# Optimization experiments

Measured on AMD Instinct MI355X. Metric: run time of the kernel, lower is better.

Reference implementation:

```python
import jax, jax.numpy as jnp
import numpy as np

N_NODES = 100000
N_EDGES = 25000
NNZ = 800000
D_IN = 256
D_OUT = 256


def setup_inputs() -> dict:
    key = jax.random.key(0)
    k1, k2, k3, k4, k5, k6, k7 = jax.random.split(key, 7)
    return {
        "input": jax.random.normal(k1, (N_NODES, D_IN), dtype=jnp.float32),
        "V": jax.random.randint(k2, (NNZ,), 0, N_NODES, dtype=jnp.int32),
        "E": jax.random.randint(k3, (NNZ,), 0, N_EDGES, dtype=jnp.int32),
        "degV": jax.random.uniform(k4, (N_NODES, 1), dtype=jnp.float32),
        "degE": jax.random.uniform(k5, (N_EDGES, 1), dtype=jnp.float32),
        "weight": jax.random.normal(k6, (D_IN, D_OUT), dtype=jnp.float32) / np.sqrt(D_OUT),
        "bias": jax.random.normal(k7, (D_OUT,), dtype=jnp.float32) / np.sqrt(D_OUT),
    }


def reference(input, V, E, degV, degE, weight, bias):
    num_nodes = degV.shape[0]
    num_edges = degE.shape[0]
    # dense projection: [N, D_in] @ [D_in, D_out]
    X = input @ weight
    # vertex -> edge: gather per-incidence node feats, scatter-mean into edges
    Xve = X[V]  # [nnz, D_out]
    esum = jax.ops.segment_sum(Xve, E, num_segments=num_edges)
    ecnt = jax.ops.segment_sum(jnp.ones((E.shape[0], 1), X.dtype), E, num_segments=num_edges)
    Xe = esum / jnp.maximum(ecnt, 1.0)  # scatter mean
    Xe = Xe * degE  # edge degree scaling
    # edge -> vertex: gather edge feats, scatter-sum into nodes
    Xev = Xe[E]  # [nnz, D_out]
    Xv = jax.ops.segment_sum(Xev, V, num_segments=num_nodes)
    return Xv * degV + bias
```

## Files before the change

kernel.cpp:

```cpp
#include <hip/hip_runtime.h>
#include <stdint.h>

#define N_NODES 100000
#define N_EDGES 25000
#define NNZ_    800000
#define D       256
#define NTOT    (N_EDGES + N_NODES)
#define SB      1024
#define NBLK    ((NTOT + SB) / SB)
#define MP      25024

#define SHE   9
#define SHV   11
#define WKE   512
#define WKV   2048
#define NBKE  ((N_EDGES + WKE - 1) / WKE)
#define NBKV  ((N_NODES + WKV - 1) / WKV)
#define NB    (NBKE + NBKV)
#define CAP   24576

#define WB 256
#define CB ((N_NODES * D / 8 + 255) / 256)

typedef short  short8   __attribute__((ext_vector_type(8)));
typedef float  f32x4    __attribute__((ext_vector_type(4)));
typedef ushort ushortx8 __attribute__((ext_vector_type(8)));
typedef ushort ushortx4 __attribute__((ext_vector_type(4)));

__device__ __forceinline__ ushort f2bf(float f) {
    uint32_t u = __float_as_uint(f);
    uint32_t r = u + 0x7fffu + ((u >> 16) & 1u);
    return (ushort)(r >> 16);
}
__device__ __forceinline__ float bf2f(ushort u) {
    return __uint_as_float(((uint32_t)u) << 16);
}


__global__ void __launch_bounds__(256) front_kernel(const float* __restrict__ W,
                                                    ushort* __restrict__ WT,
                                                    const float* __restrict__ in,
                                                    ushort* __restrict__ Xbf) {
    int b = blockIdx.x, t = threadIdx.x;
    if (b < WB) {
        int g = b * 256 + t;
        int n = g >> 8, k = g & 255;
        WT[(size_t)n * 256 + k] = f2bf(W[(size_t)k * 256 + n]);
    } else {
        int i = (b - WB) * 256 + t;
        if (i >= N_NODES * D / 8) return;
        const float4* p = reinterpret_cast<const float4*>(in) + (size_t)i * 2;
        float4 a = p[0], c = p[1];
        ushortx8 o;
        o[0] = f2bf(a.x); o[1] = f2bf(a.y); o[2] = f2bf(a.z); o[3] = f2bf(a.w);
        o[4] = f2bf(c.x); o[5] = f2bf(c.y); o[6] = f2bf(c.z); o[7] = f2bf(c.w);
        *(reinterpret_cast<ushortx8*>(Xbf) + i) = o;
    }
}


__global__ void __launch_bounds__(256) scatter1(const int* __restrict__ V,
                                                const int* __restrict__ E,
                                                int* __restrict__ gcur,
                                                int2* __restrict__ pairs) {
    __shared__ int cnt[NB], base[NB], lcur[NB];
    int t = threadIdx.x;
    for (int j = t; j < NB; j += 256) cnt[j] = 0;
    __syncthreads();
    int i0 = (blockIdx.x * 256 + t) * 16;
    bool act = i0 < NNZ_;
    if (act) {
#pragma unroll
        for (int c = 0; c < 16; c += 4) {
            int4 e = *reinterpret_cast<const int4*>(E + i0 + c);
            int4 v = *reinterpret_cast<const int4*>(V + i0 + c);
            atomicAdd(&cnt[e.x >> SHE], 1);
            atomicAdd(&cnt[e.y >> SHE], 1);
            atomicAdd(&cnt[e.z >> SHE], 1);
            atomicAdd(&cnt[e.w >> SHE], 1);
            atomicAdd(&cnt[NBKE + (v.x >> SHV)], 1);
            atomicAdd(&cnt[NBKE + (v.y >> SHV)], 1);
            atomicAdd(&cnt[NBKE + (v.z >> SHV)], 1);
            atomicAdd(&cnt[NBKE + (v.w >> SHV)], 1);
        }
    }
    __syncthreads();
    for (int j = t; j < NB; j += 256) {
        int c = cnt[j];
        base[j] = c ? atomicAdd(&gcur[j], c) : 0;
        lcur[j] = 0;
    }
    __syncthreads();
    if (act) {
#pragma unroll
        for (int c = 0; c < 16; c += 4) {
            int4 e = *reinterpret_cast<const int4*>(E + i0 + c);
            int4 v = *reinterpret_cast<const int4*>(V + i0 + c);
            int ev[4] = {e.x, e.y, e.z, e.w};
            int vv[4] = {v.x, v.y, v.z, v.w};
#pragma unroll
            for (int k = 0; k < 4; ++k) {
                int b1 = ev[k] >> SHE;
                int p1 = base[b1] + atomicAdd(&lcur[b1], 1);
                if (p1 < CAP) pairs[(size_t)b1 * CAP + p1] = make_int2(ev[k], vv[k]);
                int b2 = NBKE + (vv[k] >> SHV);
                int p2 = base[b2] + atomicAdd(&lcur[b2], 1);
                if (p2 < CAP) pairs[(size_t)b2 * CAP + p2] = make_int2(vv[k], ev[k]);
            }
        }
    }
}


__global__ void __launch_bounds__(256) count2(const int2* __restrict__ pairs,
                                              const int* __restrict__ gcur,
                                              int* __restrict__ cntC) {
    __shared__ int hist[WKV];
    int b = blockIdx.x, t = threadIdx.x;
    bool eside = b < NBKE;
    int kb    = eside ? b * WKE : (b - NBKE) * WKV;
    int wk    = eside ? WKE : WKV;
    int nk    = eside ? min(WKE, N_EDGES - kb) : min(WKV, N_NODES - kb);
    int obase = eside ? kb : N_EDGES + kb;
    for (int j = t; j < wk; j += 256) hist[j] = 0;
    __syncthreads();
    int n = min(gcur[b], CAP);
    const int2* p = pairs + (size_t)b * CAP;
    for (int i = t; i < n; i += 256) {
        int2 pr = p[i];
        atomicAdd(&hist[pr.x - kb], 1);
    }
    __syncthreads();
    for (int j = t; j < nk; j += 256) cntC[obase + j] = hist[j];
}


__global__ void __launch_bounds__(256) scan_bsum(const int* __restrict__ in,
                                                 int* __restrict__ bsum, int n) {
    __shared__ int sh[256];
    int b = blockIdx.x, t = threadIdx.x;
    int base = b * SB + t * 4;
    int s = 0;
    if (base + 4 <= n) {
        int4 v = *reinterpret_cast<const int4*>(in + base);
        s = v.x + v.y + v.z + v.w;
    } else {
        for (int k = 0; k < 4; ++k)
            if (base + k < n) s += in[base + k];
    }
    sh[t] = s;
    __syncthreads();
    for (int off = 128; off > 0; off >>= 1) {
        if (t < off) sh[t] += sh[t + off];
        __syncthreads();
    }
    if (t == 0) bsum[b] = sh[0];
}

__global__ void __launch_bounds__(128) scan_boff(int* __restrict__ bsum, int nb) {
    __shared__ int sh[128];
    int t = threadIdx.x;
    int v = (t < nb) ? bsum[t] : 0;
    sh[t] = v;
    __syncthreads();
    for (int off = 1; off < 128; off <<= 1) {
        int u = (t >= off) ? sh[t - off] : 0;
        __syncthreads();
        sh[t] += u;
        __syncthreads();
    }
    if (t < nb) bsum[t] = sh[t] - v;
}

__global__ void __launch_bounds__(256) scan_write(const int* __restrict__ in,
                                                  const int* __restrict__ bsum,
                                                  int* __restrict__ off, int n) {
    __shared__ int sh[256];
    int b = blockIdx.x, t = threadIdx.x;
    int base = b * SB + t * 4;
    int v0 = 0, v1 = 0, v2 = 0, v3 = 0;
    if (base + 4 <= n) {
        int4 v = *reinterpret_cast<const int4*>(in + base);
        v0 = v.x; v1 = v.y; v2 = v.z; v3 = v.w;
    } else {
        if (base + 0 < n) v0 = in[base + 0];
        if (base + 1 < n) v1 = in[base + 1];
        if (base + 2 < n) v2 = in[base + 2];
        if (base + 3 < n) v3 = in[base + 3];
    }
    int s = v0 + v1 + v2 + v3;
    sh[t] = s;
    __syncthreads();
    for (int o = 1; o < 256; o <<= 1) {
        int u = (t >= o) ? sh[t - o] : 0;
        __syncthreads();
        sh[t] += u;
        __syncthreads();
    }
    int excl = bsum[b] + sh[t] - s;
    if (base + 0 <= n) off[base + 0] = excl; excl += v0;
    if (base + 1 <= n) off[base + 1] = excl; excl += v1;
    if (base + 2 <= n) off[base + 2] = excl; excl += v2;
    if (base + 3 <= n) off[base + 3] = excl;
}


__global__ void __launch_bounds__(256) fill3(const int2* __restrict__ pairs,
                                             const int* __restrict__ gcur,
                                             const int* __restrict__ offC,
                                             int* __restrict__ adjAll) {
    __shared__ int cur[WKV];
    int b = blockIdx.x, t = threadIdx.x;
    bool eside = b < NBKE;
    int kb    = eside ? b * WKE : (b - NBKE) * WKV;
    int nk    = eside ? min(WKE, N_EDGES - kb) : min(WKV, N_NODES - kb);
    int obase = eside ? kb : N_EDGES + kb;
    for (int j = t; j < nk; j += 256) cur[j] = offC[obase + j];
    __syncthreads();
    int n = min(gcur[b], CAP);
    const int2* p = pairs + (size_t)b * CAP;
    for (int i = t; i < n; i += 256) {
        int2 pr = p[i];
        int slot = atomicAdd(&cur[pr.x - kb], 1);
        adjAll[slot] = pr.y;
    }
}


__global__ void edge_agg(const ushort* __restrict__ Xbf, const int* __restrict__ adjAll,
                         const int* __restrict__ offC, const float* __restrict__ degE,
                         ushort* __restrict__ Ye) {
    int gid = blockIdx.x * blockDim.x + threadIdx.x;
    int edge = gid >> 6;
    int lane = gid & 63;
    if (edge >= N_EDGES) return;
    int half = lane >> 5;
    int col8 = (lane & 31) * 8;
    int b = offC[edge], e = offC[edge + 1];
    float a[8] = {0.f, 0.f, 0.f, 0.f, 0.f, 0.f, 0.f, 0.f};
    for (int i = b; i < e; i += 2) {
        int i2 = i + half;
        bool valid = i2 < e;
        int row = adjAll[valid ? i2 : i];
        ushortx8 x = *reinterpret_cast<const ushortx8*>(Xbf + (size_t)row * D + col8);
        if (valid) {
#pragma unroll
            for (int k = 0; k < 8; ++k) a[k] += bf2f(x[k]);
        }
    }
#pragma unroll
    for (int k = 0; k < 8; ++k) a[k] += __shfl_xor(a[k], 32, 64);
    int cnt = e - b;
    float s = degE[edge] / (float)(cnt > 1 ? cnt : 1);
    int k0 = half * 4;
    ushortx4 o;
    o[0] = f2bf(a[k0 + 0] * s); o[1] = f2bf(a[k0 + 1] * s);
    o[2] = f2bf(a[k0 + 2] * s); o[3] = f2bf(a[k0 + 3] * s);
    *reinterpret_cast<ushortx4*>(Ye + (size_t)edge * D + col8 + k0) = o;
}


__global__ void __launch_bounds__(256) gemm_mfma(const ushort* __restrict__ A,
                                                 const ushort* __restrict__ WT,
                                                 ushort* __restrict__ C, int M) {
    int wid  = threadIdx.x >> 6;
    int lane = threadIdx.x & 63;
    int row0 = blockIdx.x * 64 + wid * 16;
    int lr  = lane & 15;
    int lk8 = (lane >> 4) * 8;
    f32x4 acc[16];
#pragma unroll
    for (int t = 0; t < 16; ++t) acc[t] = (f32x4){0.f, 0.f, 0.f, 0.f};
    int arow = row0 + lr;
    if (arow >= M) arow = M - 1;
    const ushort* aptr = A + (size_t)arow * D;
#pragma unroll
    for (int k0 = 0; k0 < D; k0 += 32) {
        short8 af = *reinterpret_cast<const short8*>(aptr + k0 + lk8);
#pragma unroll
        for (int t = 0; t < 16; ++t) {
            short8 bf = *reinterpret_cast<const short8*>(
                WT + (size_t)(t * 16 + lr) * D + k0 + lk8);
            acc[t] = __builtin_amdgcn_mfma_f32_16x16x32_bf16(af, bf, acc[t], 0, 0, 0);
        }
    }
    int crow = row0 + (lane >> 4) * 4;
#pragma unroll
    for (int t = 0; t < 16; ++t) {
        int ccol = t * 16 + lr;
#pragma unroll
        for (int r = 0; r < 4; ++r) {
            int rr = crow + r;
            if (rr < M) C[(size_t)rr * D + ccol] = f2bf(acc[t][r]);
        }
    }
}


__global__ void node_agg(const ushort* __restrict__ Ze, const int* __restrict__ adjAll,
                         const int* __restrict__ offC, const float* __restrict__ degV,
                         const float* __restrict__ bias, float* __restrict__ out) {
    int gid = blockIdx.x * blockDim.x + threadIdx.x;
    int node = gid >> 6;
    int lane = gid & 63;
    if (node >= N_NODES) return;
    int half = lane >> 5;
    int col8 = (lane & 31) * 8;
    int b = offC[N_EDGES + node], e = offC[N_EDGES + node + 1];
    float a[8] = {0.f, 0.f, 0.f, 0.f, 0.f, 0.f, 0.f, 0.f};
    for (int i = b; i < e; i += 2) {
        int i2 = i + half;
        bool valid = i2 < e;
        int row = adjAll[valid ? i2 : i];
        ushortx8 z = *reinterpret_cast<const ushortx8*>(Ze + (size_t)row * D + col8);
        if (valid) {
#pragma unroll
            for (int k = 0; k < 8; ++k) a[k] += bf2f(z[k]);
        }
    }
#pragma unroll
    for (int k = 0; k < 8; ++k) a[k] += __shfl_xor(a[k], 32, 64);
    float dv = degV[node];
    int k0 = half * 4;
    int c = col8 + k0;
    float4 b4 = *reinterpret_cast<const float4*>(bias + c);
    float4 o = {a[k0 + 0] * dv + b4.x, a[k0 + 1] * dv + b4.y,
                a[k0 + 2] * dv + b4.z, a[k0 + 3] * dv + b4.w};
    *reinterpret_cast<float4*>(out + (size_t)node * D + c) = o;
}


extern "C" void kernel_launch(void* const* d_in, const int* in_sizes, int n_in,
                              void* d_out, int out_size, void* d_ws, size_t ws_size,
                              hipStream_t stream) {
    const float* input  = (const float*)d_in[0];
    const int*   V      = (const int*)d_in[1];
    const int*   E      = (const int*)d_in[2];
    const float* degV   = (const float*)d_in[3];
    const float* degE   = (const float*)d_in[4];
    const float* weight = (const float*)d_in[5];
    const float* bias   = (const float*)d_in[6];
    float* out = (float*)d_out;

    int* cntC   = (int*)d_ws;
    int* gcur   = cntC + NTOT;
    int* offC   = gcur + 128;
    int* bsum   = offC + (NTOT + 1);
    int* adjAll = bsum + 128;
    uintptr_t p = (uintptr_t)(adjAll + 2 * NNZ_);
    p = (p + 255) & ~(uintptr_t)255;
    ushort* Xbf = (ushort*)p;
    ushort* Ye  = Xbf + (size_t)N_NODES * D;
    ushort* Ze  = Ye + (size_t)MP * D;
    ushort* WT  = Ze + (size_t)MP * D;
    int2* pairs = (int2*)Ye;

    hipMemsetAsync(cntC, 0, (size_t)(NTOT + 128) * sizeof(int), stream);

    front_kernel<<<WB + CB, 256, 0, stream>>>(weight, WT, input, Xbf);

    scatter1<<<(NNZ_ / 16 + 255) / 256, 256, 0, stream>>>(V, E, gcur, pairs);
    count2<<<NB, 256, 0, stream>>>(pairs, gcur, cntC);
    scan_bsum<<<NBLK, 256, 0, stream>>>(cntC, bsum, NTOT);
    scan_boff<<<1, 128, 0, stream>>>(bsum, NBLK);
    scan_write<<<NBLK, 256, 0, stream>>>(cntC, bsum, offC, NTOT);
    fill3<<<NB, 256, 0, stream>>>(pairs, gcur, offC, adjAll);

    edge_agg<<<(N_EDGES * 64 + 255) / 256, 256, 0, stream>>>(Xbf, adjAll, offC, degE, Ye);

    gemm_mfma<<<MP / 64, 256, 0, stream>>>(Ye, WT, Ze, N_EDGES);

    node_agg<<<(N_NODES * 64 + 255) / 256, 256, 0, stream>>>(Ze, adjAll, offC, degV, bias, out);
}
```

Before: 273.0 us.

## Fuse bucket scatter into front kernel, unroll gathers, use nontemporal loads/stores

Merges the incidence bucketing (scatter1) into the front conversion kernel as extra blocks, so bucketing runs alongside the weight transpose and input bf16 conversion in one launch. The edge and node aggregation loops are unrolled to issue two row gathers per half-wave per iteration, raising memory-level parallelism. Nontemporal loads are used for the input conversion and nontemporal stores for the final output. Every block of the fused kernel now reserves the scatter's shared memory, which may lower occupancy for the conversion blocks. The unrolled loops also use more registers.

```diff
diff --git a/kernel.cpp b/kernel.cpp
--- a/kernel.cpp
+++ b/kernel.cpp
@@ -19,6 +19,7 @@
 #define NB    (NBKE + NBKV)
 #define CAP   24576
 
+#define SC1B ((NNZ_ / 16 + 255) / 256)
 #define WB 256
 #define CB ((N_NODES * D / 8 + 255) / 256)
 
@@ -37,77 +38,75 @@
 }
 
 
-__global__ void __launch_bounds__(256) front_kernel(const float* __restrict__ W,
+__global__ void __launch_bounds__(256) front_kernel(const int* __restrict__ V,
+                                                    const int* __restrict__ E,
+                                                    int* __restrict__ gcur,
+                                                    int2* __restrict__ pairs,
+                                                    const float* __restrict__ W,
                                                     ushort* __restrict__ WT,
                                                     const float* __restrict__ in,
                                                     ushort* __restrict__ Xbf) {
-    int b = blockIdx.x, t = threadIdx.x;
-    if (b < WB) {
-        int g = b * 256 + t;
+    __shared__ int cnt[NB], base[NB], lcur[NB];
+    int b = blockIdx.x, t = threadIdx.x;
+    if (b < SC1B) {
+        for (int j = t; j < NB; j += 256) cnt[j] = 0;
+        __syncthreads();
+        int i0 = (b * 256 + t) * 16;
+        bool act = i0 < NNZ_;
+        if (act) {
+#pragma unroll
+            for (int c = 0; c < 16; c += 4) {
+                int4 e = *reinterpret_cast<const int4*>(E + i0 + c);
+                int4 v = *reinterpret_cast<const int4*>(V + i0 + c);
+                atomicAdd(&cnt[e.x >> SHE], 1);
+                atomicAdd(&cnt[e.y >> SHE], 1);
+                atomicAdd(&cnt[e.z >> SHE], 1);
+                atomicAdd(&cnt[e.w >> SHE], 1);
+                atomicAdd(&cnt[NBKE + (v.x >> SHV)], 1);
+                atomicAdd(&cnt[NBKE + (v.y >> SHV)], 1);
+                atomicAdd(&cnt[NBKE + (v.z >> SHV)], 1);
+                atomicAdd(&cnt[NBKE + (v.w >> SHV)], 1);
+            }
+        }
+        __syncthreads();
+        for (int j = t; j < NB; j += 256) {
+            int c = cnt[j];
+            base[j] = c ? atomicAdd(&gcur[j], c) : 0;
+            lcur[j] = 0;
+        }
+        __syncthreads();
+        if (act) {
+#pragma unroll
+            for (int c = 0; c < 16; c += 4) {
+                int4 e = *reinterpret_cast<const int4*>(E + i0 + c);
+                int4 v = *reinterpret_cast<const int4*>(V + i0 + c);
+                int ev[4] = {e.x, e.y, e.z, e.w};
+                int vv[4] = {v.x, v.y, v.z, v.w};
+#pragma unroll
+                for (int k = 0; k < 4; ++k) {
+                    int b1 = ev[k] >> SHE;
+                    int p1 = base[b1] + atomicAdd(&lcur[b1], 1);
+                    if (p1 < CAP) pairs[(size_t)b1 * CAP + p1] = make_int2(ev[k], vv[k]);
+                    int b2 = NBKE + (vv[k] >> SHV);
+                    int p2 = base[b2] + atomicAdd(&lcur[b2], 1);
+                    if (p2 < CAP) pairs[(size_t)b2 * CAP + p2] = make_int2(vv[k], ev[k]);
+                }
+            }
+        }
+    } else if (b < SC1B + WB) {
+        int g = (b - SC1B) * 256 + t;
         int n = g >> 8, k = g & 255;
         WT[(size_t)n * 256 + k] = f2bf(W[(size_t)k * 256 + n]);
     } else {
-        int i = (b - WB) * 256 + t;
+        int i = (b - SC1B - WB) * 256 + t;
         if (i >= N_NODES * D / 8) return;
-        const float4* p = reinterpret_cast<const float4*>(in) + (size_t)i * 2;
-        float4 a = p[0], c = p[1];
+        const f32x4* p = reinterpret_cast<const f32x4*>(in) + (size_t)i * 2;
+        f32x4 a = __builtin_nontemporal_load(p);
+        f32x4 c = __builtin_nontemporal_load(p + 1);
         ushortx8 o;
-        o[0] = f2bf(a.x); o[1] = f2bf(a.y); o[2] = f2bf(a.z); o[3] = f2bf(a.w);
-        o[4] = f2bf(c.x); o[5] = f2bf(c.y); o[6] = f2bf(c.z); o[7] = f2bf(c.w);
+        o[0] = f2bf(a[0]); o[1] = f2bf(a[1]); o[2] = f2bf(a[2]); o[3] = f2bf(a[3]);
+        o[4] = f2bf(c[0]); o[5] = f2bf(c[1]); o[6] = f2bf(c[2]); o[7] = f2bf(c[3]);
         *(reinterpret_cast<ushortx8*>(Xbf) + i) = o;
-    }
-}
-
-
-__global__ void __launch_bounds__(256) scatter1(const int* __restrict__ V,
-                                                const int* __restrict__ E,
-                                                int* __restrict__ gcur,
-                                                int2* __restrict__ pairs) {
-    __shared__ int cnt[NB], base[NB], lcur[NB];
-    int t = threadIdx.x;
-    for (int j = t; j < NB; j += 256) cnt[j] = 0;
-    __syncthreads();
-    int i0 = (blockIdx.x * 256 + t) * 16;
-    bool act = i0 < NNZ_;
-    if (act) {
-#pragma unroll
-        for (int c = 0; c < 16; c += 4) {
-            int4 e = *reinterpret_cast<const int4*>(E + i0 + c);
-            int4 v = *reinterpret_cast<const int4*>(V + i0 + c);
-            atomicAdd(&cnt[e.x >> SHE], 1);
-            atomicAdd(&cnt[e.y >> SHE], 1);
-            atomicAdd(&cnt[e.z >> SHE], 1);
-            atomicAdd(&cnt[e.w >> SHE], 1);
-            atomicAdd(&cnt[NBKE + (v.x >> SHV)], 1);
-            atomicAdd(&cnt[NBKE + (v.y >> SHV)], 1);
-            atomicAdd(&cnt[NBKE + (v.z >> SHV)], 1);
-            atomicAdd(&cnt[NBKE + (v.w >> SHV)], 1);
-        }
-    }
-    __syncthreads();
-    for (int j = t; j < NB; j += 256) {
-        int c = cnt[j];
-        base[j] = c ? atomicAdd(&gcur[j], c) : 0;
-        lcur[j] = 0;
-    }
-    __syncthreads();
-    if (act) {
-#pragma unroll
-        for (int c = 0; c < 16; c += 4) {
-            int4 e = *reinterpret_cast<const int4*>(E + i0 + c);
-            int4 v = *reinterpret_cast<const int4*>(V + i0 + c);
-            int ev[4] = {e.x, e.y, e.z, e.w};
-            int vv[4] = {v.x, v.y, v.z, v.w};
-#pragma unroll
-            for (int k = 0; k < 4; ++k) {
-                int b1 = ev[k] >> SHE;
-                int p1 = base[b1] + atomicAdd(&lcur[b1], 1);
-                if (p1 < CAP) pairs[(size_t)b1 * CAP + p1] = make_int2(ev[k], vv[k]);
-                int b2 = NBKE + (vv[k] >> SHV);
-                int p2 = base[b2] + atomicAdd(&lcur[b2], 1);
-                if (p2 < CAP) pairs[(size_t)b2 * CAP + p2] = make_int2(vv[k], ev[k]);
-            }
-        }
     }
 }
 
@@ -238,14 +237,20 @@
     int col8 = (lane & 31) * 8;
     int b = offC[edge], e = offC[edge + 1];
     float a[8] = {0.f, 0.f, 0.f, 0.f, 0.f, 0.f, 0.f, 0.f};
-    for (int i = b; i < e; i += 2) {
-        int i2 = i + half;
-        bool valid = i2 < e;
-        int row = adjAll[valid ? i2 : i];
-        ushortx8 x = *reinterpret_cast<const ushortx8*>(Xbf + (size_t)row * D + col8);
-        if (valid) {
-#pragma unroll
-            for (int k = 0; k < 8; ++k) a[k] += bf2f(x[k]);
+    for (int i = b; i < e; i += 4) {
+        int ia = i + half, ib = i + 2 + half;
+        bool va = ia < e, vb = ib < e;
+        int ra = adjAll[va ? ia : b];
+        int rb = adjAll[vb ? ib : b];
+        ushortx8 xa = *reinterpret_cast<const ushortx8*>(Xbf + (size_t)ra * D + col8);
+        ushortx8 xb = *reinterpret_cast<const ushortx8*>(Xbf + (size_t)rb * D + col8);
+        if (va) {
+#pragma unroll
+            for (int k = 0; k < 8; ++k) a[k] += bf2f(xa[k]);
+        }
+        if (vb) {
+#pragma unroll
+            for (int k = 0; k < 8; ++k) a[k] += bf2f(xb[k]);
         }
     }
 #pragma unroll
@@ -308,14 +313,20 @@
     int col8 = (lane & 31) * 8;
     int b = offC[N_EDGES + node], e = offC[N_EDGES + node + 1];
     float a[8] = {0.f, 0.f, 0.f, 0.f, 0.f, 0.f, 0.f, 0.f};
-    for (int i = b; i < e; i += 2) {
-        int i2 = i + half;
-        bool valid = i2 < e;
-        int row = adjAll[valid ? i2 : i];
-        ushortx8 z = *reinterpret_cast<const ushortx8*>(Ze + (size_t)row * D + col8);
-        if (valid) {
-#pragma unroll
-            for (int k = 0; k < 8; ++k) a[k] += bf2f(z[k]);
+    for (int i = b; i < e; i += 4) {
+        int ia = i + half, ib = i + 2 + half;
+        bool va = ia < e, vb = ib < e;
+        int ra = adjAll[va ? ia : b];
+        int rb = adjAll[vb ? ib : b];
+        ushortx8 za = *reinterpret_cast<const ushortx8*>(Ze + (size_t)ra * D + col8);
+        ushortx8 zb = *reinterpret_cast<const ushortx8*>(Ze + (size_t)rb * D + col8);
+        if (va) {
+#pragma unroll
+            for (int k = 0; k < 8; ++k) a[k] += bf2f(za[k]);
+        }
+        if (vb) {
+#pragma unroll
+            for (int k = 0; k < 8; ++k) a[k] += bf2f(zb[k]);
         }
     }
 #pragma unroll
@@ -323,10 +334,14 @@
     float dv = degV[node];
     int k0 = half * 4;
     int c = col8 + k0;
-    float4 b4 = *reinterpret_cast<const float4*>(bias + c);
-    float4 o = {a[k0 + 0] * dv + b4.x, a[k0 + 1] * dv + b4.y,
-                a[k0 + 2] * dv + b4.z, a[k0 + 3] * dv + b4.w};
-    *reinterpret_cast<float4*>(out + (size_t)node * D + c) = o;
+    const f32x4* bp = reinterpret_cast<const f32x4*>(bias + c);
+    f32x4 b4 = *bp;
+    f32x4 o;
+    o[0] = a[k0 + 0] * dv + b4[0];
+    o[1] = a[k0 + 1] * dv + b4[1];
+    o[2] = a[k0 + 2] * dv + b4[2];
+    o[3] = a[k0 + 3] * dv + b4[3];
+    __builtin_nontemporal_store(o, reinterpret_cast<f32x4*>(out + (size_t)node * D + c));
 }
 
 
@@ -357,9 +372,9 @@
 
     hipMemsetAsync(cntC, 0, (size_t)(NTOT + 128) * sizeof(int), stream);
 
-    front_kernel<<<WB + CB, 256, 0, stream>>>(weight, WT, input, Xbf);
-
-    scatter1<<<(NNZ_ / 16 + 255) / 256, 256, 0, stream>>>(V, E, gcur, pairs);
+    front_kernel<<<SC1B + WB + CB, 256, 0, stream>>>(V, E, gcur, pairs,
+                                                     weight, WT, input, Xbf);
+
     count2<<<NB, 256, 0, stream>>>(pairs, gcur, cntC);
     scan_bsum<<<NBLK, 256, 0, stream>>>(cntC, bsum, NTOT);
     scan_boff<<<1, 128, 0, stream>>>(bsum, NBLK);
```

After: 262.8 us. -3.7%, faster.
